# Kernel tuning notes

Hardware: AMD Instinct MI355X
Metric: run time of the kernel (lower is better)

## Reference

```python
import jax, jax.numpy as jnp
import numpy as np

N_NODES = 50000
N_EDGES = 800000


def _graph_conv(feature, W, b, src, dst, edge_w, n_nodes, activation=None):
    # DGL GraphConv, norm='both', with edge_weight.
    ones = jnp.ones((src.shape[0],), dtype=feature.dtype)
    deg_out = jnp.clip(jax.ops.segment_sum(ones, src, num_segments=n_nodes), 1.0)
    deg_in = jnp.clip(jax.ops.segment_sum(ones, dst, num_segments=n_nodes), 1.0)
    # scale src side by out-deg^-1/2, transform first (in_feats > out_feats path)
    h = (feature * (deg_out ** -0.5)[:, None]) @ W            # [N, out]
    msgs = h[src] * edge_w[:, None]                            # [E, out]
    agg = jax.ops.segment_sum(msgs, dst, num_segments=n_nodes) # [N, out]
    out = agg * (deg_in ** -0.5)[:, None] + b
    if activation is not None:
        out = activation(out)
    return out


def setup_inputs() -> dict:
    key = jax.random.key(0)
    ks = jax.random.split(key, 8)
    feature = jax.random.normal(ks[0], (N_NODES, 768), dtype=jnp.float32)
    src = jax.random.randint(ks[1], (N_EDGES,), 0, N_NODES, dtype=jnp.int32)
    dst = jax.random.randint(ks[2], (N_EDGES,), 0, N_NODES, dtype=jnp.int32)
    edge_w = jax.random.uniform(ks[3], (N_EDGES,), dtype=jnp.float32)
    W1 = jax.random.normal(ks[4], (768, 200), dtype=jnp.float32) * (768 ** -0.5)
    b1 = jnp.zeros((200,), dtype=jnp.float32)
    W2 = jax.random.normal(ks[5], (200, 20), dtype=jnp.float32) * (200 ** -0.5)
    b2 = jnp.zeros((20,), dtype=jnp.float32)
    return {"feature": feature, "src": src, "dst": dst, "edge_w": edge_w,
            "W1": W1, "b1": b1, "W2": W2, "b2": b2}


def reference(feature, src, dst, edge_w, W1, b1, W2, b2):
    n = feature.shape[0]
    # dropout layers are identity in eval mode
    h = _graph_conv(feature, W1, b1, src, dst, edge_w, n, activation=jax.nn.relu)
    out = _graph_conv(h, W2, b2, src, dst, edge_w, n)
    return out
```

## Files before the change

kernel.cpp:

```cpp
#include <hip/hip_runtime.h>

#define N_NODES 50000
#define N_EDGES 800000
#define F_IN 768
#define H1 200
#define H1P 208
#define H2 20
#define NB_SCAN 196
#define NT 13

typedef unsigned short ushort_t;
typedef __attribute__((ext_vector_type(8))) short bf16x8;
typedef __attribute__((ext_vector_type(4))) float f32x4;


__global__ __launch_bounds__(256) void k_count(const int* __restrict__ src,
                                               const int* __restrict__ dst,
                                               int* __restrict__ cnt_src,
                                               int* __restrict__ cnt_dst) {
  int i = blockIdx.x * 256 + threadIdx.x;
  if (i < N_EDGES) {
    atomicAdd(&cnt_src[src[i]], 1);
    atomicAdd(&cnt_dst[dst[i]], 1);
  }
}

__global__ __launch_bounds__(256) void k_scan_block(const int* __restrict__ cnt_dst,
                                                    int* __restrict__ row_start,
                                                    int* __restrict__ partials) {
  __shared__ int sm[256];
  int i = blockIdx.x * 256 + threadIdx.x;
  int v = (i < N_NODES) ? cnt_dst[i] : 0;
  sm[threadIdx.x] = v;
  __syncthreads();
#pragma unroll
  for (int off = 1; off < 256; off <<= 1) {
    int t = (threadIdx.x >= off) ? sm[threadIdx.x - off] : 0;
    __syncthreads();
    sm[threadIdx.x] += t;
    __syncthreads();
  }
  if (i < N_NODES) row_start[i] = sm[threadIdx.x] - v;
  if (threadIdx.x == 255) partials[blockIdx.x] = sm[255];
}

__global__ __launch_bounds__(256) void k_scan_partials(int* __restrict__ partials) {
  __shared__ int sm[256];
  int v = (threadIdx.x < NB_SCAN) ? partials[threadIdx.x] : 0;
  sm[threadIdx.x] = v;
  __syncthreads();
#pragma unroll
  for (int off = 1; off < 256; off <<= 1) {
    int t = (threadIdx.x >= off) ? sm[threadIdx.x - off] : 0;
    __syncthreads();
    sm[threadIdx.x] += t;
    __syncthreads();
  }
  partials[threadIdx.x] = sm[threadIdx.x] - v;
}

__global__ __launch_bounds__(256) void k_scan_add(const int* __restrict__ cnt_dst,
                                                  const int* __restrict__ cnt_src,
                                                  const int* __restrict__ partials,
                                                  int* __restrict__ row_start,
                                                  float* __restrict__ dinv_in,
                                                  float* __restrict__ dinv_out) {
  int i = blockIdx.x * 256 + threadIdx.x;
  if (i < N_NODES) {
    row_start[i] += partials[blockIdx.x];
    dinv_in[i] = rsqrtf(fmaxf((float)cnt_dst[i], 1.f));
    dinv_out[i] = rsqrtf(fmaxf((float)cnt_src[i], 1.f));
  }
}

__global__ __launch_bounds__(256) void k_fill(const int* __restrict__ src,
                                              const int* __restrict__ dst,
                                              const float* __restrict__ ew,
                                              const int* __restrict__ row_start,
                                              int* __restrict__ cursor,
                                              int* __restrict__ src_s,
                                              float* __restrict__ w_s) {
  int e = blockIdx.x * 256 + threadIdx.x;
  if (e < N_EDGES) {
    int d = dst[e];
    int pos = atomicAdd(&cursor[d], 1);
    int idx = row_start[d] + pos;
    src_s[idx] = src[e];
    w_s[idx] = ew[e];
  }
}

__global__ __launch_bounds__(256) void k_splitW(const float* __restrict__ W1,
                                                ushort_t* __restrict__ WH,
                                                ushort_t* __restrict__ WL) {
  int idx = blockIdx.x * 256 + threadIdx.x;
  if (idx >= 208 * F_IN) return;
  int col = idx / F_IN, k = idx % F_IN;
  float f = (col < H1) ? W1[k * H1 + col] : 0.f;
  unsigned b = __float_as_uint(f);
  unsigned h = b >> 16;
  float lo = f - __uint_as_float(h << 16);
  WH[idx] = (ushort_t)h;
  WL[idx] = (ushort_t)(__float_as_uint(lo) >> 16);
}

__global__ __launch_bounds__(256) void k_gemm1_mfma(
    const float* __restrict__ A,
    const ushort_t* __restrict__ BH,
    const ushort_t* __restrict__ BL,
    const float* __restrict__ dinv_out,
    float* __restrict__ H) {
  __shared__ ushort_t AsH[32][32];
  __shared__ ushort_t AsL[32][32];
  __shared__ ushort_t BsH[NT][16][32];
  __shared__ ushort_t BsL[NT][16][32];

  const int t = threadIdx.x;
  const int wid = t >> 6;
  const int lane = t & 63;
  const int bm = blockIdx.x * 32;

  const bool astage = t < 128;
  const int arow = t >> 2;
  const int akq = t & 3;
  const int aslot = (akq + ((arow >> 1) & 3)) & 3;
  const int agr = bm + arow;
  const float* __restrict__ arowp = &A[(size_t)agr * F_IN + akq * 8];

  const int frow = lane & 15;
  const int kq = lane >> 4;
  const int wm = wid & 1;
  const int wn = wid >> 1;
  const int ntbase = wn * 7;
  const int ntcnt = wn ? 6 : 7;
  const int row_local = wm * 16 + frow;
  const int arslot = (kq + ((row_local >> 1) & 3)) & 3;
  const int brslot = (kq + ((frow >> 1) & 3)) & 3;

  const int bf = lane >> 2;
  const int bq = ((lane & 3) - ((lane >> 3) & 3)) & 3;

  f32x4 acc[7];
#pragma unroll
  for (int i = 0; i < 7; ++i) acc[i] = (f32x4)(0.f);

  float4 v0 = make_float4(0.f, 0.f, 0.f, 0.f), v1 = v0;
  if (astage && agr < N_NODES) {
    v0 = *(const float4*)&arowp[0];
    v1 = *(const float4*)&arowp[4];
  }

  for (int k0 = 0; k0 < F_IN; k0 += 32) {
    float fv[8] = {v0.x, v0.y, v0.z, v0.w, v1.x, v1.y, v1.z, v1.w};
    unsigned hp[4], lp[4];
#pragma unroll
    for (int i = 0; i < 4; ++i) {
      unsigned b0 = __float_as_uint(fv[2 * i]);
      unsigned b1 = __float_as_uint(fv[2 * i + 1]);
      unsigned h0 = b0 >> 16, h1 = b1 >> 16;
      float lo0 = fv[2 * i] - __uint_as_float(h0 << 16);
      float lo1 = fv[2 * i + 1] - __uint_as_float(h1 << 16);
      hp[i] = h0 | (h1 << 16);
      lp[i] = (__float_as_uint(lo0) >> 16) | (__float_as_uint(lo1) & 0xffff0000u);
    }

    __syncthreads();

    if (astage) {
      *(uint4*)&AsH[arow][aslot * 8] = make_uint4(hp[0], hp[1], hp[2], hp[3]);
      *(uint4*)&AsL[arow][aslot * 8] = make_uint4(lp[0], lp[1], lp[2], lp[3]);
    }

    for (int nt = wid; nt < NT; nt += 4) {
      const ushort_t* gh = &BH[(size_t)(nt * 16 + bf) * F_IN + k0 + bq * 8];
      const ushort_t* gl = &BL[(size_t)(nt * 16 + bf) * F_IN + k0 + bq * 8];
      __builtin_amdgcn_global_load_lds(gh, &BsH[nt][0][0], 16, 0, 0);
      __builtin_amdgcn_global_load_lds(gl, &BsL[nt][0][0], 16, 0, 0);
    }

    v0 = make_float4(0.f, 0.f, 0.f, 0.f);
    v1 = v0;
    if (k0 + 32 < F_IN && astage && agr < N_NODES) {
      v0 = *(const float4*)&arowp[k0 + 32];
      v1 = *(const float4*)&arowp[k0 + 36];
    }

    __syncthreads();

    bf16x8 aH = *(const bf16x8*)&AsH[row_local][arslot * 8];
    bf16x8 aL = *(const bf16x8*)&AsL[row_local][arslot * 8];
#pragma unroll
    for (int i = 0; i < 7; ++i) {
      if (i >= ntcnt) break;
      int nt = ntbase + i;
      bf16x8 bH = *(const bf16x8*)&BsH[nt][frow][brslot * 8];
      bf16x8 bL = *(const bf16x8*)&BsL[nt][frow][brslot * 8];
      acc[i] = __builtin_amdgcn_mfma_f32_16x16x32_bf16(aH, bH, acc[i], 0, 0, 0);
      acc[i] = __builtin_amdgcn_mfma_f32_16x16x32_bf16(aH, bL, acc[i], 0, 0, 0);
      acc[i] = __builtin_amdgcn_mfma_f32_16x16x32_bf16(aL, bH, acc[i], 0, 0, 0);
    }
  }

  const int r0 = bm + wm * 16 + kq * 4;
  float dsc[4];
#pragma unroll
  for (int r = 0; r < 4; ++r)
    dsc[r] = (r0 + r < N_NODES) ? dinv_out[r0 + r] : 0.f;
#pragma unroll
  for (int i = 0; i < 7; ++i) {
    if (i >= ntcnt) break;
    int gc = (ntbase + i) * 16 + frow;
#pragma unroll
    for (int r = 0; r < 4; ++r) {
      int gr = r0 + r;
      if (gr < N_NODES) H[(size_t)gr * H1P + gc] = acc[i][r] * dsc[r];
    }
  }
}

__global__ __launch_bounds__(256) void k_layer1(
    const int* __restrict__ row_start, const int* __restrict__ cnt,
    const int* __restrict__ src_s, const float* __restrict__ w_s,
    const float* __restrict__ H, const float* __restrict__ dinv_in,
    const float* __restrict__ dinv_out, const float* __restrict__ b1,
    const float* __restrict__ W2, float* __restrict__ G) {
  __shared__ float Tsm[4][H1];
  const int wid = threadIdx.x >> 6;
  const int lane = threadIdx.x & 63;
  const int node = __builtin_amdgcn_readfirstlane(blockIdx.x * 4 + wid);
  const int start = __builtin_amdgcn_readfirstlane(row_start[node]);
  const int n = __builtin_amdgcn_readfirstlane(cnt[node]);
  const float4* __restrict__ Hv = (const float4*)H;
  const bool act = lane < (H1 / 4);
  float4 acc = make_float4(0.f, 0.f, 0.f, 0.f);

  int e = 0;
  for (; e + 2 <= n; e += 2) {
    int s0 = src_s[start + e];
    int s1 = src_s[start + e + 1];
    float w0 = w_s[start + e];
    float w1 = w_s[start + e + 1];
    if (act) {
      float4 u0 = Hv[(size_t)s0 * (H1P / 4) + lane];
      float4 u1 = Hv[(size_t)s1 * (H1P / 4) + lane];
      acc.x = fmaf(w0, u0.x, acc.x);
      acc.y = fmaf(w0, u0.y, acc.y);
      acc.z = fmaf(w0, u0.z, acc.z);
      acc.w = fmaf(w0, u0.w, acc.w);
      acc.x = fmaf(w1, u1.x, acc.x);
      acc.y = fmaf(w1, u1.y, acc.y);
      acc.z = fmaf(w1, u1.z, acc.z);
      acc.w = fmaf(w1, u1.w, acc.w);
    }
  }
  if (e < n) {
    int s0 = src_s[start + e];
    float w0 = w_s[start + e];
    if (act) {
      float4 u0 = Hv[(size_t)s0 * (H1P / 4) + lane];
      acc.x = fmaf(w0, u0.x, acc.x);
      acc.y = fmaf(w0, u0.y, acc.y);
      acc.z = fmaf(w0, u0.z, acc.z);
      acc.w = fmaf(w0, u0.w, acc.w);
    }
  }

  if (act) {
    float di = dinv_in[node];
    float dn = dinv_out[node];
    float4 bb = ((const float4*)b1)[lane];
    float4 r;
    r.x = fmaxf(fmaf(acc.x, di, bb.x), 0.f) * dn;
    r.y = fmaxf(fmaf(acc.y, di, bb.y), 0.f) * dn;
    r.z = fmaxf(fmaf(acc.z, di, bb.z), 0.f) * dn;
    r.w = fmaxf(fmaf(acc.w, di, bb.w), 0.f) * dn;
    *(float4*)&Tsm[wid][lane * 4] = r;
  }
  __syncthreads();

  if (lane < H2) {
    float a = 0.f;
#pragma unroll 8
    for (int d = 0; d < H1; ++d) a = fmaf(Tsm[wid][d], W2[d * H2 + lane], a);
    G[node * H2 + lane] = a;
  }
}

__global__ __launch_bounds__(256) void k_agg2_final(
    const int* __restrict__ row_start, const int* __restrict__ cnt,
    const int* __restrict__ src_s, const float* __restrict__ w_s,
    const float* __restrict__ G, const float* __restrict__ dinv_in,
    const float* __restrict__ b2, float* __restrict__ out) {
  int gi = blockIdx.x * 256 + threadIdx.x;
  if (gi >= N_NODES * H2) return;
  int node = gi / H2;
  int dim = gi % H2;
  int start = row_start[node];
  int n = cnt[node];
  float acc = 0.f;
  int e = 0;
  for (; e + 2 <= n; e += 2) {
    int s0 = src_s[start + e];
    int s1 = src_s[start + e + 1];
    float w0 = w_s[start + e];
    float w1 = w_s[start + e + 1];
    float g0 = G[s0 * H2 + dim];
    float g1 = G[s1 * H2 + dim];
    acc = fmaf(w0, g0, acc);
    acc = fmaf(w1, g1, acc);
  }
  if (e < n) {
    int s0 = src_s[start + e];
    acc = fmaf(w_s[start + e], G[s0 * H2 + dim], acc);
  }
  out[gi] = fmaf(acc, dinv_in[node], b2[dim]);
}

extern "C" void kernel_launch(void* const* d_in, const int* in_sizes, int n_in,
                              void* d_out, int out_size, void* d_ws, size_t ws_size,
                              hipStream_t stream) {
  const float* feature = (const float*)d_in[0];
  const int* src = (const int*)d_in[1];
  const int* dst = (const int*)d_in[2];
  const float* edge_w = (const float*)d_in[3];
  const float* W1 = (const float*)d_in[4];
  const float* b1 = (const float*)d_in[5];
  const float* W2 = (const float*)d_in[6];
  const float* b2 = (const float*)d_in[7];
  float* out = (float*)d_out;

  char* wsb = (char*)d_ws;
  int* cnt_dst = (int*)(wsb + 0);
  int* cnt_src = (int*)(wsb + 200000);
  int* cursor = (int*)(wsb + 400000);
  int* partials = (int*)(wsb + 600000);
  int* row_start = (int*)(wsb + 601024);
  float* dinv_in = (float*)(wsb + 801024);
  float* dinv_out = (float*)(wsb + 1001024);
  int* src_s = (int*)(wsb + 1201024);
  float* w_s = (float*)(wsb + 4401024);
  float* h = (float*)(wsb + 7601024);
  float* g2 = (float*)(wsb + 49201024);
  ushort_t* W1sH = (ushort_t*)(wsb + 53201024);
  ushort_t* W1sL = (ushort_t*)(wsb + 53520512);

  hipMemsetAsync(wsb, 0, 600000, stream);

  k_count<<<(N_EDGES + 255) / 256, 256, 0, stream>>>(src, dst, cnt_src, cnt_dst);
  k_scan_block<<<NB_SCAN, 256, 0, stream>>>(cnt_dst, row_start, partials);
  k_scan_partials<<<1, 256, 0, stream>>>(partials);
  k_scan_add<<<NB_SCAN, 256, 0, stream>>>(cnt_dst, cnt_src, partials, row_start,
                                          dinv_in, dinv_out);
  k_fill<<<(N_EDGES + 255) / 256, 256, 0, stream>>>(src, dst, edge_w, row_start,
                                                    cursor, src_s, w_s);
  k_splitW<<<(208 * F_IN + 255) / 256, 256, 0, stream>>>(W1, W1sH, W1sL);

  k_gemm1_mfma<<<(N_NODES + 31) / 32, 256, 0, stream>>>(feature, W1sH, W1sL,
                                                        dinv_out, h);

  k_layer1<<<N_NODES / 4, 256, 0, stream>>>(row_start, cnt_dst, src_s, w_s, h,
                                            dinv_in, dinv_out, b1, W2, g2);
  k_agg2_final<<<(N_NODES * H2 + 255) / 256, 256, 0, stream>>>(
      row_start, cnt_dst, src_s, w_s, g2, dinv_in, b2, out);
}
```

Baseline: 604.4 us.

## Pre-swizzle W1 into MFMA fragment layout and stream GEMM without LDS

The W1 split kernel now writes hi/lo bf16 fragments directly in the per-lane MFMA operand order. The first-layer GEMM becomes a single-wave block that loads A straight into registers and reads B fragments from global/L2 with no shared memory or barriers. Each wave computes a 32x208 tile with 26 accumulators. This removes LDS staging and syncthreads, but raises register pressure and relies on L2 to serve the B fragments re-read by every block.

```diff
diff --git a/kernel.cpp b/kernel.cpp
--- a/kernel.cpp
+++ b/kernel.cpp
@@ -8,6 +8,7 @@
 #define H2 20
 #define NB_SCAN 196
 #define NT 13
+#define KSTEPS 24
 
 typedef unsigned short ushort_t;
 typedef __attribute__((ext_vector_type(8))) short bf16x8;
@@ -91,129 +92,123 @@
 }
 
 __global__ __launch_bounds__(256) void k_splitW(const float* __restrict__ W1,
-                                                ushort_t* __restrict__ WH,
-                                                ushort_t* __restrict__ WL) {
+                                                uint4* __restrict__ Bf) {
   int idx = blockIdx.x * 256 + threadIdx.x;
-  if (idx >= 208 * F_IN) return;
-  int col = idx / F_IN, k = idx % F_IN;
-  float f = (col < H1) ? W1[k * H1 + col] : 0.f;
-  unsigned b = __float_as_uint(f);
-  unsigned h = b >> 16;
-  float lo = f - __uint_as_float(h << 16);
-  WH[idx] = (ushort_t)h;
-  WL[idx] = (ushort_t)(__float_as_uint(lo) >> 16);
-}
-
-__global__ __launch_bounds__(256) void k_gemm1_mfma(
+  if (idx >= KSTEPS * NT * 64) return;
+  int lane = idx & 63;
+  int tile = idx >> 6;
+  int nt = tile % NT;
+  int col = nt * 16 + (lane & 15);
+  int k0 = (tile / NT) * 32 + (lane >> 4) * 8;
+  unsigned hi[4], lo[4];
+#pragma unroll
+  for (int e = 0; e < 4; ++e) {
+    float f0 = (col < H1) ? W1[(k0 + 2 * e) * H1 + col] : 0.f;
+    float f1 = (col < H1) ? W1[(k0 + 2 * e + 1) * H1 + col] : 0.f;
+    unsigned h0 = __float_as_uint(f0) >> 16;
+    unsigned h1 = __float_as_uint(f1) >> 16;
+    float l0 = f0 - __uint_as_float(h0 << 16);
+    float l1 = f1 - __uint_as_float(h1 << 16);
+    hi[e] = h0 | (h1 << 16);
+    lo[e] = (__float_as_uint(l0) >> 16) | (__float_as_uint(l1) & 0xffff0000u);
+  }
+  uint4* p = &Bf[(size_t)(tile * 2) * 64 + lane];
+  p[0] = make_uint4(hi[0], hi[1], hi[2], hi[3]);
+  p[64] = make_uint4(lo[0], lo[1], lo[2], lo[3]);
+}
+
+__global__ __launch_bounds__(64) void k_gemm1_stream(
     const float* __restrict__ A,
-    const ushort_t* __restrict__ BH,
-    const ushort_t* __restrict__ BL,
+    const uint4* __restrict__ Bf,
     const float* __restrict__ dinv_out,
     float* __restrict__ H) {
-  __shared__ ushort_t AsH[32][32];
-  __shared__ ushort_t AsL[32][32];
-  __shared__ ushort_t BsH[NT][16][32];
-  __shared__ ushort_t BsL[NT][16][32];
-
-  const int t = threadIdx.x;
-  const int wid = t >> 6;
-  const int lane = t & 63;
+  const int lane = threadIdx.x;
   const int bm = blockIdx.x * 32;
-
-  const bool astage = t < 128;
-  const int arow = t >> 2;
-  const int akq = t & 3;
-  const int aslot = (akq + ((arow >> 1) & 3)) & 3;
-  const int agr = bm + arow;
-  const float* __restrict__ arowp = &A[(size_t)agr * F_IN + akq * 8];
-
-  const int frow = lane & 15;
+  const int fr = lane & 15;
   const int kq = lane >> 4;
-  const int wm = wid & 1;
-  const int wn = wid >> 1;
-  const int ntbase = wn * 7;
-  const int ntcnt = wn ? 6 : 7;
-  const int row_local = wm * 16 + frow;
-  const int arslot = (kq + ((row_local >> 1) & 3)) & 3;
-  const int brslot = (kq + ((frow >> 1) & 3)) & 3;
-
-  const int bf = lane >> 2;
-  const int bq = ((lane & 3) - ((lane >> 3) & 3)) & 3;
-
-  f32x4 acc[7];
-#pragma unroll
-  for (int i = 0; i < 7; ++i) acc[i] = (f32x4)(0.f);
-
-  float4 v0 = make_float4(0.f, 0.f, 0.f, 0.f), v1 = v0;
-  if (astage && agr < N_NODES) {
-    v0 = *(const float4*)&arowp[0];
-    v1 = *(const float4*)&arowp[4];
-  }
-
-  for (int k0 = 0; k0 < F_IN; k0 += 32) {
-    float fv[8] = {v0.x, v0.y, v0.z, v0.w, v1.x, v1.y, v1.z, v1.w};
-    unsigned hp[4], lp[4];
-#pragma unroll
-    for (int i = 0; i < 4; ++i) {
+
+  const int ar0 = bm + fr;
+  const int ar1 = bm + 16 + fr;
+  const bool ok0 = ar0 < N_NODES;
+  const bool ok1 = ar1 < N_NODES;
+  const float* __restrict__ pa0 = &A[(size_t)ar0 * F_IN + kq * 8];
+  const float* __restrict__ pa1 = &A[(size_t)ar1 * F_IN + kq * 8];
+
+  f32x4 acc0[NT], acc1[NT];
+#pragma unroll
+  for (int i = 0; i < NT; ++i) {
+    acc0[i] = (f32x4)(0.f);
+    acc1[i] = (f32x4)(0.f);
+  }
+
+  const float4 fz = make_float4(0.f, 0.f, 0.f, 0.f);
+  float4 va0 = ok0 ? *(const float4*)(pa0) : fz;
+  float4 va1 = ok0 ? *(const float4*)(pa0 + 4) : fz;
+  float4 va2 = ok1 ? *(const float4*)(pa1) : fz;
+  float4 va3 = ok1 ? *(const float4*)(pa1 + 4) : fz;
+
+  for (int ks = 0; ks < KSTEPS; ++ks) {
+    float fv[16] = {va0.x, va0.y, va0.z, va0.w, va1.x, va1.y, va1.z, va1.w,
+                    va2.x, va2.y, va2.z, va2.w, va3.x, va3.y, va3.z, va3.w};
+    unsigned hp[8], lp[8];
+#pragma unroll
+    for (int i = 0; i < 8; ++i) {
       unsigned b0 = __float_as_uint(fv[2 * i]);
       unsigned b1 = __float_as_uint(fv[2 * i + 1]);
       unsigned h0 = b0 >> 16, h1 = b1 >> 16;
-      float lo0 = fv[2 * i] - __uint_as_float(h0 << 16);
-      float lo1 = fv[2 * i + 1] - __uint_as_float(h1 << 16);
+      float l0 = fv[2 * i] - __uint_as_float(h0 << 16);
+      float l1 = fv[2 * i + 1] - __uint_as_float(h1 << 16);
       hp[i] = h0 | (h1 << 16);
-      lp[i] = (__float_as_uint(lo0) >> 16) | (__float_as_uint(lo1) & 0xffff0000u);
-    }
-
-    __syncthreads();
-
-    if (astage) {
-      *(uint4*)&AsH[arow][aslot * 8] = make_uint4(hp[0], hp[1], hp[2], hp[3]);
-      *(uint4*)&AsL[arow][aslot * 8] = make_uint4(lp[0], lp[1], lp[2], lp[3]);
-    }
-
-    for (int nt = wid; nt < NT; nt += 4) {
-      const ushort_t* gh = &BH[(size_t)(nt * 16 + bf) * F_IN + k0 + bq * 8];
-      const ushort_t* gl = &BL[(size_t)(nt * 16 + bf) * F_IN + k0 + bq * 8];
-      __builtin_amdgcn_global_load_lds(gh, &BsH[nt][0][0], 16, 0, 0);
-      __builtin_amdgcn_global_load_lds(gl, &BsL[nt][0][0], 16, 0, 0);
-    }
-
-    v0 = make_float4(0.f, 0.f, 0.f, 0.f);
-    v1 = v0;
-    if (k0 + 32 < F_IN && astage && agr < N_NODES) {
-      v0 = *(const float4*)&arowp[k0 + 32];
-      v1 = *(const float4*)&arowp[k0 + 36];
-    }
-
-    __syncthreads();
-
-    bf16x8 aH = *(const bf16x8*)&AsH[row_local][arslot * 8];
-    bf16x8 aL = *(const bf16x8*)&AsL[row_local][arslot * 8];
-#pragma unroll
-    for (int i = 0; i < 7; ++i) {
-      if (i >= ntcnt) break;
-      int nt = ntbase + i;
-      bf16x8 bH = *(const bf16x8*)&BsH[nt][frow][brslot * 8];
-      bf16x8 bL = *(const bf16x8*)&BsL[nt][frow][brslot * 8];
-      acc[i] = __builtin_amdgcn_mfma_f32_16x16x32_bf16(aH, bH, acc[i], 0, 0, 0);
-      acc[i] = __builtin_amdgcn_mfma_f32_16x16x32_bf16(aH, bL, acc[i], 0, 0, 0);
-      acc[i] = __builtin_amdgcn_mfma_f32_16x16x32_bf16(aL, bH, acc[i], 0, 0, 0);
-    }
-  }
-
-  const int r0 = bm + wm * 16 + kq * 4;
-  float dsc[4];
-#pragma unroll
-  for (int r = 0; r < 4; ++r)
-    dsc[r] = (r0 + r < N_NODES) ? dinv_out[r0 + r] : 0.f;
-#pragma unroll
-  for (int i = 0; i < 7; ++i) {
-    if (i >= ntcnt) break;
-    int gc = (ntbase + i) * 16 + frow;
-#pragma unroll
-    for (int r = 0; r < 4; ++r) {
-      int gr = r0 + r;
-      if (gr < N_NODES) H[(size_t)gr * H1P + gc] = acc[i][r] * dsc[r];
+      lp[i] = (__float_as_uint(l0) >> 16) | (__float_as_uint(l1) & 0xffff0000u);
+    }
+    uint4 uH0 = make_uint4(hp[0], hp[1], hp[2], hp[3]);
+    uint4 uL0 = make_uint4(lp[0], lp[1], lp[2], lp[3]);
+    uint4 uH1 = make_uint4(hp[4], hp[5], hp[6], hp[7]);
+    uint4 uL1 = make_uint4(lp[4], lp[5], lp[6], lp[7]);
+    bf16x8 aH0 = *(bf16x8*)&uH0;
+    bf16x8 aL0 = *(bf16x8*)&uL0;
+    bf16x8 aH1 = *(bf16x8*)&uH1;
+    bf16x8 aL1 = *(bf16x8*)&uL1;
+
+    if (ks + 1 < KSTEPS) {
+      int o = (ks + 1) * 32;
+      va0 = ok0 ? *(const float4*)(pa0 + o) : fz;
+      va1 = ok0 ? *(const float4*)(pa0 + o + 4) : fz;
+      va2 = ok1 ? *(const float4*)(pa1 + o) : fz;
+      va3 = ok1 ? *(const float4*)(pa1 + o + 4) : fz;
+    }
+
+    const uint4* __restrict__ bp = Bf + (size_t)(ks * NT * 2) * 64 + lane;
+#pragma unroll
+    for (int nt = 0; nt < NT; ++nt) {
+      bf16x8 bH = *(const bf16x8*)&bp[nt * 128];
+      bf16x8 bL = *(const bf16x8*)&bp[nt * 128 + 64];
+      acc0[nt] = __builtin_amdgcn_mfma_f32_16x16x32_bf16(aH0, bH, acc0[nt], 0, 0, 0);
+      acc0[nt] = __builtin_amdgcn_mfma_f32_16x16x32_bf16(aH0, bL, acc0[nt], 0, 0, 0);
+      acc0[nt] = __builtin_amdgcn_mfma_f32_16x16x32_bf16(aL0, bH, acc0[nt], 0, 0, 0);
+      acc1[nt] = __builtin_amdgcn_mfma_f32_16x16x32_bf16(aH1, bH, acc1[nt], 0, 0, 0);
+      acc1[nt] = __builtin_amdgcn_mfma_f32_16x16x32_bf16(aH1, bL, acc1[nt], 0, 0, 0);
+      acc1[nt] = __builtin_amdgcn_mfma_f32_16x16x32_bf16(aL1, bH, acc1[nt], 0, 0, 0);
+    }
+  }
+
+  float d0[4], d1[4];
+#pragma unroll
+  for (int rr = 0; rr < 4; ++rr) {
+    int g0 = bm + kq * 4 + rr;
+    int g1 = bm + 16 + kq * 4 + rr;
+    d0[rr] = (g0 < N_NODES) ? dinv_out[g0] : 0.f;
+    d1[rr] = (g1 < N_NODES) ? dinv_out[g1] : 0.f;
+  }
+#pragma unroll
+  for (int nt = 0; nt < NT; ++nt) {
+    int gc = nt * 16 + fr;
+#pragma unroll
+    for (int rr = 0; rr < 4; ++rr) {
+      int g0 = bm + kq * 4 + rr;
+      int g1 = bm + 16 + kq * 4 + rr;
+      if (g0 < N_NODES) H[(size_t)g0 * H1P + gc] = acc0[nt][rr] * d0[rr];
+      if (g1 < N_NODES) H[(size_t)g1 * H1P + gc] = acc1[nt][rr] * d1[rr];
     }
   }
 }
@@ -341,8 +336,7 @@
   float* w_s = (float*)(wsb + 4401024);
   float* h = (float*)(wsb + 7601024);
   float* g2 = (float*)(wsb + 49201024);
-  ushort_t* W1sH = (ushort_t*)(wsb + 53201024);
-  ushort_t* W1sL = (ushort_t*)(wsb + 53520512);
+  uint4* Bf = (uint4*)(wsb + 53201024);
 
   hipMemsetAsync(wsb, 0, 600000, stream);
 
@@ -353,10 +347,9 @@
                                           dinv_in, dinv_out);
   k_fill<<<(N_EDGES + 255) / 256, 256, 0, stream>>>(src, dst, edge_w, row_start,
                                                     cursor, src_s, w_s);
-  k_splitW<<<(208 * F_IN + 255) / 256, 256, 0, stream>>>(W1, W1sH, W1sL);
-
-  k_gemm1_mfma<<<(N_NODES + 31) / 32, 256, 0, stream>>>(feature, W1sH, W1sL,
-                                                        dinv_out, h);
+  k_splitW<<<(KSTEPS * NT * 64 + 255) / 256, 256, 0, stream>>>(W1, Bf);
+
+  k_gemm1_stream<<<(N_NODES + 31) / 32, 64, 0, stream>>>(feature, Bf, dinv_out, h);
 
   k_layer1<<<N_NODES / 4, 256, 0, stream>>>(row_start, cnt_dst, src_s, w_s, h,
                                             dinv_in, dinv_out, b1, W2, g2);
```

Measured after the change: 627.6 us. 3.8% more time.

## Enlarge GEMM1 row tile to 64 with each wave owning all column tiles

Applied to the files above, without the earlier changes.

The first-layer MFMA GEMM now processes 64 rows per block instead of 32. Each of the four waves owns 16 rows and computes all 13 column tiles, instead of splitting columns across wave pairs. All 256 threads now stage A, which halves the number of W1 tile loads per output row and improves B reuse from shared memory. The cost is more accumulator registers per wave (13 f32x4), which may lower occupancy, and fewer blocks overall.

```diff
diff --git a/kernel.cpp b/kernel.cpp
--- a/kernel.cpp
+++ b/kernel.cpp
@@ -110,17 +110,16 @@
     const ushort_t* __restrict__ BL,
     const float* __restrict__ dinv_out,
     float* __restrict__ H) {
-  __shared__ ushort_t AsH[32][32];
-  __shared__ ushort_t AsL[32][32];
+  __shared__ ushort_t AsH[64][32];
+  __shared__ ushort_t AsL[64][32];
   __shared__ ushort_t BsH[NT][16][32];
   __shared__ ushort_t BsL[NT][16][32];
 
   const int t = threadIdx.x;
   const int wid = t >> 6;
   const int lane = t & 63;
-  const int bm = blockIdx.x * 32;
-
-  const bool astage = t < 128;
+  const int bm = blockIdx.x * 64;
+
   const int arow = t >> 2;
   const int akq = t & 3;
   const int aslot = (akq + ((arow >> 1) & 3)) & 3;
@@ -129,23 +128,20 @@
 
   const int frow = lane & 15;
   const int kq = lane >> 4;
-  const int wm = wid & 1;
-  const int wn = wid >> 1;
-  const int ntbase = wn * 7;
-  const int ntcnt = wn ? 6 : 7;
-  const int row_local = wm * 16 + frow;
+  const int row_local = wid * 16 + frow;
   const int arslot = (kq + ((row_local >> 1) & 3)) & 3;
   const int brslot = (kq + ((frow >> 1) & 3)) & 3;
 
   const int bf = lane >> 2;
   const int bq = ((lane & 3) - ((lane >> 3) & 3)) & 3;
 
-  f32x4 acc[7];
-#pragma unroll
-  for (int i = 0; i < 7; ++i) acc[i] = (f32x4)(0.f);
-
-  float4 v0 = make_float4(0.f, 0.f, 0.f, 0.f), v1 = v0;
-  if (astage && agr < N_NODES) {
+  f32x4 acc[NT];
+#pragma unroll
+  for (int i = 0; i < NT; ++i) acc[i] = (f32x4)(0.f);
+
+  const float4 fz = make_float4(0.f, 0.f, 0.f, 0.f);
+  float4 v0 = fz, v1 = fz;
+  if (agr < N_NODES) {
     v0 = *(const float4*)&arowp[0];
     v1 = *(const float4*)&arowp[4];
   }
@@ -166,10 +162,8 @@
 
     __syncthreads();
 
-    if (astage) {
-      *(uint4*)&AsH[arow][aslot * 8] = make_uint4(hp[0], hp[1], hp[2], hp[3]);
-      *(uint4*)&AsL[arow][aslot * 8] = make_uint4(lp[0], lp[1], lp[2], lp[3]);
-    }
+    *(uint4*)&AsH[arow][aslot * 8] = make_uint4(hp[0], hp[1], hp[2], hp[3]);
+    *(uint4*)&AsL[arow][aslot * 8] = make_uint4(lp[0], lp[1], lp[2], lp[3]);
 
     for (int nt = wid; nt < NT; nt += 4) {
       const ushort_t* gh = &BH[(size_t)(nt * 16 + bf) * F_IN + k0 + bq * 8];
@@ -178,9 +172,9 @@
       __builtin_amdgcn_global_load_lds(gl, &BsL[nt][0][0], 16, 0, 0);
     }
 
-    v0 = make_float4(0.f, 0.f, 0.f, 0.f);
-    v1 = v0;
-    if (k0 + 32 < F_IN && astage && agr < N_NODES) {
+    v0 = fz;
+    v1 = fz;
+    if (k0 + 32 < F_IN && agr < N_NODES) {
       v0 = *(const float4*)&arowp[k0 + 32];
       v1 = *(const float4*)&arowp[k0 + 36];
     }
@@ -190,30 +184,27 @@
     bf16x8 aH = *(const bf16x8*)&AsH[row_local][arslot * 8];
     bf16x8 aL = *(const bf16x8*)&AsL[row_local][arslot * 8];
 #pragma unroll
-    for (int i = 0; i < 7; ++i) {
-      if (i >= ntcnt) break;
-      int nt = ntbase + i;
+    for (int nt = 0; nt < NT; ++nt) {
       bf16x8 bH = *(const bf16x8*)&BsH[nt][frow][brslot * 8];
       bf16x8 bL = *(const bf16x8*)&BsL[nt][frow][brslot * 8];
-      acc[i] = __builtin_amdgcn_mfma_f32_16x16x32_bf16(aH, bH, acc[i], 0, 0, 0);
-      acc[i] = __builtin_amdgcn_mfma_f32_16x16x32_bf16(aH, bL, acc[i], 0, 0, 0);
-      acc[i] = __builtin_amdgcn_mfma_f32_16x16x32_bf16(aL, bH, acc[i], 0, 0, 0);
-    }
-  }
-
-  const int r0 = bm + wm * 16 + kq * 4;
+      acc[nt] = __builtin_amdgcn_mfma_f32_16x16x32_bf16(aH, bH, acc[nt], 0, 0, 0);
+      acc[nt] = __builtin_amdgcn_mfma_f32_16x16x32_bf16(aH, bL, acc[nt], 0, 0, 0);
+      acc[nt] = __builtin_amdgcn_mfma_f32_16x16x32_bf16(aL, bH, acc[nt], 0, 0, 0);
+    }
+  }
+
+  const int r0 = bm + wid * 16 + kq * 4;
   float dsc[4];
 #pragma unroll
   for (int r = 0; r < 4; ++r)
     dsc[r] = (r0 + r < N_NODES) ? dinv_out[r0 + r] : 0.f;
 #pragma unroll
-  for (int i = 0; i < 7; ++i) {
-    if (i >= ntcnt) break;
-    int gc = (ntbase + i) * 16 + frow;
+  for (int nt = 0; nt < NT; ++nt) {
+    int gc = nt * 16 + frow;
 #pragma unroll
     for (int r = 0; r < 4; ++r) {
       int gr = r0 + r;
-      if (gr < N_NODES) H[(size_t)gr * H1P + gc] = acc[i][r] * dsc[r];
+      if (gr < N_NODES) H[(size_t)gr * H1P + gc] = acc[nt][r] * dsc[r];
     }
   }
 }
@@ -355,7 +346,7 @@
                                                     cursor, src_s, w_s);
   k_splitW<<<(208 * F_IN + 255) / 256, 256, 0, stream>>>(W1, W1sH, W1sL);
 
-  k_gemm1_mfma<<<(N_NODES + 31) / 32, 256, 0, stream>>>(feature, W1sH, W1sL,
+  k_gemm1_mfma<<<(N_NODES + 63) / 64, 256, 0, stream>>>(feature, W1sH, W1sL,
                                                         dinv_out, h);
 
   k_layer1<<<N_NODES / 4, 256, 0, stream>>>(row_start, cnt_dst, src_s, w_s, h,
```

New measurement: 582.8 us. 1.04x faster.
